# Kernel tuning notes

Measured on AMD Instinct MI355X. Metric: run time of the kernel, lower is better.

## Reference

```python
import jax, jax.numpy as jnp
import numpy as np

V = 128   # vocab / number of symbols (len(index_map))
N = 512   # number of automaton states
L = 4096  # input string length


def setup_inputs() -> dict:
    key = jax.random.key(0)
    k0, k1, k2, k3, k4 = jax.random.split(key, 5)
    tokens = jax.random.randint(k0, (L,), 0, V, dtype=jnp.int32)
    # start distribution over states
    start = jax.nn.softmax(jax.random.normal(k1, (N,), dtype=jnp.float32))
    # row-stochastic transition matrices, one per symbol: [V, N, N]
    transfer = jax.nn.softmax(jax.random.normal(k2, (V, N, N), dtype=jnp.float32), axis=-1)
    # per-symbol prob vectors near 1.0 so the running product stays finite: [V, N]
    probs = 0.9 + 0.2 * jax.random.uniform(k3, (V, N), dtype=jnp.float32)
    # final acceptance vector: [N]
    finals = jax.random.uniform(k4, (N,), dtype=jnp.float32)
    return {"tokens": tokens, "start": start, "transfer": transfer,
            "probs": probs, "finals": finals}


def reference(tokens, start, transfer, probs, finals):
    # Faithful device-side version of the Python loop:
    #   prob *= internal @ prob_tensors[sym]; internal = internal @ transfer_tensors[sym]
    # index_map is identity (symbol == tensor index). Whole walk is one lax.scan,
    # removing the per-step host sync of the original.
    def step(carry, t):
        internal, prob = carry
        prob = prob * jnp.dot(internal, probs[t])          # scalar emission prob
        internal = jnp.dot(internal, transfer[t])          # [N] @ [N,N] -> [N]
        return (internal, prob), None

    init = (start, jnp.float32(1.0))
    (internal, prob), _ = jax.lax.scan(step, init, tokens)
    prob = prob * jnp.dot(internal, finals)
    return internal, prob
```

## Files before the change

### kernel.cpp

```cpp
#include <hip/hip_runtime.h>
#include <stdint.h>


typedef unsigned short ushort_t;
typedef __attribute__((ext_vector_type(8))) short v8s;
typedef __attribute__((ext_vector_type(4))) float f32x4;

#define NSTATE 512
#define NSYM   128
#define LTOK   4096
#define MS     ((size_t)NSTATE*NSTATE)

__device__ __forceinline__ ushort_t f2bf(float f){
  unsigned u = __float_as_uint(f);
  u = u + 0x7FFFu + ((u >> 16) & 1u);
  return (ushort_t)(u >> 16);
}
__device__ __forceinline__ float bf2f(ushort_t h){
  return __uint_as_float(((unsigned)h) << 16);
}
__device__ __forceinline__ size_t fragT_idx(int m, int k){
  return ((size_t)((k >> 5)*512 + m)*4 + ((k >> 3) & 3))*8 + (k & 7);
}

__device__ __forceinline__ void step_mfma64(f32x4 acc[4][4],
    const ushort_t* __restrict__ As, const ushort_t* __restrict__ Bf,
    int wv, int l15, int q4){
  const ushort_t* base = Bf + ((size_t)(wv*64 + l15)*4 + q4)*8;
  v8s aA[4], aN[4];
  #pragma unroll
  for (int mt = 0; mt < 4; ++mt) aA[mt] = *(const v8s*)&base[mt*512];
  #pragma unroll
  for (int kk = 0; kk < 16; ++kk){
    if (kk < 15){
      #pragma unroll
      for (int mt = 0; mt < 4; ++mt)
        aN[mt] = *(const v8s*)&base[(size_t)(kk+1)*16384 + mt*512];
    }
    #pragma unroll
    for (int nt = 0; nt < 4; ++nt){
      int n  = nt*16 + l15;
      int ch = kk*4 + q4;
      v8s bf = *(const v8s*)&As[n*512 + ((ch ^ (n & 7))*8)];
      #pragma unroll
      for (int mt = 0; mt < 4; ++mt)
        acc[mt][nt] = __builtin_amdgcn_mfma_f32_16x16x32_bf16(aA[mt], bf, acc[mt][nt], 0,0,0);
    }
    #pragma unroll
    for (int mt = 0; mt < 4; ++mt) aA[mt] = aN[mt];
  }
}

__device__ __forceinline__ void load_strip64(ushort_t* As,
    const ushort_t* __restrict__ src, int rowbase, int tid){
  #pragma unroll
  for (int q = 0; q < 8; ++q){
    int F = tid + q*512;
    int m = F >> 6, p = F & 63;
    *(v8s*)&As[m*512 + p*8] =
      *(const v8s*)&src[(size_t)(rowbase + m)*NSTATE + ((p ^ (m & 7))*8)];
  }
}

__device__ __forceinline__ void writeback64(ushort_t* As, f32x4 acc[4][4],
    int wv, int l15, int q4){
  #pragma unroll
  for (int nt = 0; nt < 4; ++nt){
    int n = nt*16 + l15;
    #pragma unroll
    for (int mt = 0; mt < 4; ++mt){
      int col = wv*64 + mt*16 + q4*4;
      ushort4 h;
      h.x = f2bf(acc[mt][nt][0]); h.y = f2bf(acc[mt][nt][1]);
      h.z = f2bf(acc[mt][nt][2]); h.w = f2bf(acc[mt][nt][3]);
      int p = (col >> 3) ^ (n & 7);
      *(ushort4*)&As[n*512 + p*8 + (col & 7)] = h;
    }
  }
}

__device__ __forceinline__ void store_out64(ushort_t* slot, f32x4 acc[4][4],
    int rowbase, bool even, int lane, int wv, int l15, int q4){
  if (even){
    #pragma unroll
    for (int nt = 0; nt < 4; ++nt){
      int grow = rowbase + nt*16 + l15;
      #pragma unroll
      for (int mt = 0; mt < 4; ++mt){
        int gcol = wv*64 + mt*16 + q4*4;
        ushort4 h;
        h.x = f2bf(acc[mt][nt][0]); h.y = f2bf(acc[mt][nt][1]);
        h.z = f2bf(acc[mt][nt][2]); h.w = f2bf(acc[mt][nt][3]);
        *(ushort4*)&slot[(size_t)grow*NSTATE + gcol] = h;
      }
    }
  } else {
    #pragma unroll
    for (int nt = 0; nt < 4; ++nt){
      int G0 = rowbase + nt*16 + (l15 & 12);
      #pragma unroll
      for (int mt = 0; mt < 4; ++mt){
        float v0 = acc[mt][nt][0], v1 = acc[mt][nt][1];
        float v2 = acc[mt][nt][2], v3 = acc[mt][nt][3];
        float s0 = __shfl_xor(v0, 2), s1 = __shfl_xor(v1, 2);
        float s2 = __shfl_xor(v2, 2), s3 = __shfl_xor(v3, 2);
        const bool h2 = lane & 2;
        float c0 = h2 ? s2 : v0, c1 = h2 ? s3 : v1;
        float c2 = h2 ? v2 : s0, c3 = h2 ? v3 : s1;
        float u0 = __shfl_xor(c0, 1), u1 = __shfl_xor(c1, 1);
        float u2 = __shfl_xor(c2, 1), u3 = __shfl_xor(c3, 1);
        const bool h1 = lane & 1;
        float d0 = h1 ? u1 : c0, d1 = h1 ? c1 : u0;
        float d2 = h1 ? u3 : c2, d3 = h1 ? c3 : u2;
        int mcol = wv*64 + mt*16 + q4*4 + (lane & 3);
        ushort4 h;
        h.x = f2bf(d0); h.y = f2bf(d1); h.z = f2bf(d2); h.w = f2bf(d3);
        *(ushort4*)&slot[fragT_idx(mcol, G0)] = h;
      }
    }
  }
}

__global__ __launch_bounds__(512, 4) void k_chain3(
    const int* __restrict__ tokens, const ushort_t* __restrict__ Tb,
    const ushort_t* __restrict__ Tf, ushort_t* __restrict__ Lout, int W){
  extern __shared__ __align__(16) ushort_t As[];
  const int b = blockIdx.x;
  const int c       = (b >> 6) * 8 + (b & 7);
  const int rowbase = ((b >> 3) & 7) * 64;
  const int tid  = threadIdx.x;
  const int lane = tid & 63;
  const int wv   = tid >> 6;
  const int l15  = lane & 15;
  const int q4   = lane >> 4;
  const int t0   = c * W;

  load_strip64(As, Tb + (size_t)tokens[t0] * MS, rowbase, tid);
  __syncthreads();
  for (int k = 1; k < W; ++k){
    f32x4 acc[4][4];
    #pragma unroll
    for (int mt = 0; mt < 4; ++mt)
      #pragma unroll
      for (int nt = 0; nt < 4; ++nt) acc[mt][nt] = (f32x4){0.f,0.f,0.f,0.f};
    step_mfma64(acc, As, Tf + (size_t)tokens[t0 + k] * MS, wv, l15, q4);
    __syncthreads();
    if (k < W - 1){
      writeback64(As, acc, wv, l15, q4);
      __syncthreads();
    } else {
      store_out64(Lout + (size_t)c * MS, acc, rowbase, !(c & 1), lane, wv, l15, q4);
    }
  }
}

__global__ __launch_bounds__(512, 4) void k_tree3(
    const ushort_t* __restrict__ Lsrc, ushort_t* __restrict__ Ldst){
  extern __shared__ __align__(16) ushort_t As[];
  const int b = blockIdx.x;
  int j, strip;
  if (gridDim.x >= 64){ j = (b >> 6) * 8 + (b & 7); strip = (b >> 3) & 7; }
  else                { j = b >> 3;                  strip = b & 7; }
  const int rowbase = strip * 64;
  const int tid  = threadIdx.x;
  const int lane = tid & 63;
  const int wv   = tid >> 6;
  const int l15  = lane & 15;
  const int q4   = lane >> 4;
  load_strip64(As, Lsrc + (size_t)(2*j) * MS, rowbase, tid);
  __syncthreads();
  f32x4 acc[4][4];
  #pragma unroll
  for (int mt = 0; mt < 4; ++mt)
    #pragma unroll
    for (int nt = 0; nt < 4; ++nt) acc[mt][nt] = (f32x4){0.f,0.f,0.f,0.f};
  step_mfma64(acc, As, Lsrc + (size_t)(2*j + 1) * MS, wv, l15, q4);
  store_out64(Ldst + (size_t)j * MS, acc, rowbase, !(j & 1), lane, wv, l15, q4);
}

__global__ __launch_bounds__(256) void k_prep(const float* __restrict__ transfer,
                                              ushort_t* __restrict__ Tb,
                                              ushort_t* __restrict__ Tf){
  __shared__ ushort_t t[32*512];
  const int s = blockIdx.x >> 4;
  const int kk = blockIdx.x & 15;
  const int krows = kk * 32;
  const int tid = threadIdx.x;
  for (int idx = tid; idx < 32*512; idx += 256){
    int r = idx >> 9, n = idx & 511;
    ushort_t h = f2bf(transfer[(size_t)s*MS + (size_t)(krows + r)*NSTATE + n]);
    Tb[(size_t)s*MS + (size_t)(krows + r)*NSTATE + n] = h;
    t[r*512 + n] = h;
  }
  __syncthreads();
  for (int idx = tid; idx < 512*4; idx += 256){
    int n = idx >> 2, cc = idx & 3;
    v8s vv;
    #pragma unroll
    for (int jj = 0; jj < 8; ++jj) vv[jj] = (short)t[(cc*8 + jj)*512 + n];
    *(v8s*)&Tf[(size_t)s*MS + ((size_t)(kk*512 + n)*4 + cc)*8] = vv;
  }
}

__device__ __forceinline__ void gl_lds16(const void* g, void* l){
  __builtin_amdgcn_global_load_lds(
      (const __attribute__((address_space(1))) unsigned int*)g,
      (__attribute__((address_space(3))) unsigned int*)l, 16, 0, 0);
}

__device__ void gemm_step(const ushort_t* __restrict__ A,
                          const ushort_t* __restrict__ Bf,
                          ushort_t* dRM, ushort_t* dT, int rowbase){
  __shared__ __align__(16) ushort_t ldsA[128*64];
  __shared__ __align__(16) ushort_t ldsB[128*64];
  const int tid  = threadIdx.x;
  const int lane = tid & 63;
  const int w    = tid >> 6;
  const int l15  = lane & 15;
  const int koff = (lane >> 4) * 8;

  __threadfence_block();

  for (int p = 0; p < 4; ++p){
    f32x4 acc[2][8];
    #pragma unroll
    for (int rt = 0; rt < 2; ++rt)
      #pragma unroll
      for (int ct = 0; ct < 8; ++ct) acc[rt][ct] = (f32x4){0.f,0.f,0.f,0.f};

    for (int kk = 0; kk < 8; ++kk){
      __syncthreads();
      #pragma unroll
      for (int q = 0; q < 4; ++q){
        int idx = tid + q*256;
        int rr = idx >> 3, cch = idx & 7;
        gl_lds16(&A [(size_t)(rowbase + rr)*NSTATE + kk*64 + cch*8], &ldsA[idx*8]);
        gl_lds16(&Bf[fragT_idx(p*128 + rr, kk*64 + cch*8)], &ldsB[idx*8]);
      }
      __syncthreads();
      #pragma unroll
      for (int kc = 0; kc < 2; ++kc){
        v8s a0 = *(const v8s*)&ldsA[(w*32 +      l15)*64 + kc*32 + koff];
        v8s a1 = *(const v8s*)&ldsA[(w*32 + 16 + l15)*64 + kc*32 + koff];
        #pragma unroll
        for (int ct = 0; ct < 8; ++ct){
          v8s bb = *(const v8s*)&ldsB[(ct*16 + l15)*64 + kc*32 + koff];
          acc[0][ct] = __builtin_amdgcn_mfma_f32_16x16x32_bf16(a0, bb, acc[0][ct], 0,0,0);
          acc[1][ct] = __builtin_amdgcn_mfma_f32_16x16x32_bf16(a1, bb, acc[1][ct], 0,0,0);
        }
      }
    }
    const int rb = rowbase + w*32 + (lane >> 4)*4;
    #pragma unroll
    for (int rt = 0; rt < 2; ++rt)
      #pragma unroll
      for (int ct = 0; ct < 8; ++ct)
        #pragma unroll
        for (int i = 0; i < 4; ++i){
          int grow = rb + rt*16 + i;
          int gcol = p*128 + ct*16 + l15;
          ushort_t h = f2bf(acc[rt][ct][i]);
          if (dRM) dRM[(size_t)grow*NSTATE + gcol] = h;
          if (dT)  dT [fragT_idx(gcol, grow)] = h;
        }
  }
  __syncthreads();
}

__global__ __launch_bounds__(256) void k_chain(const int* __restrict__ tokens,
    const ushort_t* __restrict__ Tb, const ushort_t* __restrict__ Tf,
    ushort_t* ping, ushort_t* pong, ushort_t* Lout, int W){
  const int c = blockIdx.x >> 2;
  const int r = blockIdx.x & 3;
  const int t0 = c * W;
  ushort_t* bufA = ping + (size_t)c * MS;
  ushort_t* bufB = pong + (size_t)c * MS;
  for (int k = 1; k < W; ++k){
    const ushort_t* Asrc = (k == 1) ? Tb + (size_t)tokens[t0] * MS
                                    : (((k - 1) & 1) ? bufA : bufB);
    ushort_t *dRM, *dT;
    if (k == W - 1){
      ushort_t* slot = Lout + (size_t)c * MS;
      dRM = (c & 1) ? nullptr : slot;
      dT  = (c & 1) ? slot    : nullptr;
    } else {
      dRM = (k & 1) ? bufA : bufB; dT = nullptr;
    }
    gemm_step(Asrc, Tf + (size_t)tokens[t0 + k] * MS, dRM, dT, r * 128);
  }
}

__global__ __launch_bounds__(256) void k_tree(const ushort_t* __restrict__ Lsrc,
                                              ushort_t* __restrict__ Ldst){
  const int j = blockIdx.x >> 2, r = blockIdx.x & 3;
  const ushort_t* A  = Lsrc + (size_t)(2*j)     * MS;
  const ushort_t* Bf = Lsrc + (size_t)(2*j + 1) * MS;
  ushort_t* slot = Ldst + (size_t)j * MS;
  gemm_step(A, Bf, (j & 1) ? nullptr : slot, (j & 1) ? slot : nullptr, r * 128);
}

__global__ __launch_bounds__(512) void k_descent(const float* __restrict__ start,
    const ushort_t* __restrict__ lvl4, const ushort_t* __restrict__ Upper,
    float* __restrict__ u, int baseLvl){
  __shared__ float v[NSTATE];
  const int upOff[7] = {0,128,192,224,240,248,252};
  const int g = blockIdx.x, tid = threadIdx.x;
  v[tid] = start[tid];
  __syncthreads();
  int pos = 0;
  for (int p = 11 - baseLvl; p >= 0; --p){
    if ((g >> p) & 1){
      const int L = baseLvl + p;
      const ushort_t* arr = (L == 4) ? lvl4 : (Upper + (size_t)upOff[L-5] * MS);
      const ushort_t* M = arr + (size_t)(pos >> p) * MS;
      float a0=0.f,a1=0.f,a2=0.f,a3=0.f;
      #pragma unroll 4
      for (int i = 0; i < NSTATE; i += 4){
        a0 += v[i  ] * bf2f(M[(size_t)(i  )*NSTATE + tid]);
        a1 += v[i+1] * bf2f(M[(size_t)(i+1)*NSTATE + tid]);
        a2 += v[i+2] * bf2f(M[(size_t)(i+2)*NSTATE + tid]);
        a3 += v[i+3] * bf2f(M[(size_t)(i+3)*NSTATE + tid]);
      }
      __syncthreads();
      v[tid] = (a0+a1)+(a2+a3);
      __syncthreads();
      pos += 1 << p;
    }
  }
  u[(size_t)g*NSTATE + tid] = v[tid];
}

__global__ __launch_bounds__(512) void k_phase2(const int* __restrict__ tokens,
    const float* __restrict__ u, const ushort_t* __restrict__ Tf,
    const float* __restrict__ probs, float* __restrict__ partials,
    float* __restrict__ out, int SEG){
  __shared__ float v[NSTATE];
  __shared__ float redc[8], redm[8];
  __shared__ float fac, minv;
  const int g = blockIdx.x, tid = threadIdx.x;
  v[tid] = u[(size_t)g*NSTATE + tid];
  float pp = 1.f;
  __syncthreads();
  for (int k = 0; k < SEG; ++k){
    const int tok = tokens[g*SEG + k];
    float a = v[tid];
    float bb = a * probs[(size_t)tok*NSTATE + tid];
    #pragma unroll
    for (int o = 32; o > 0; o >>= 1){
      a  += __shfl_down(a, o);
      bb += __shfl_down(bb, o);
    }
    if ((tid & 63) == 0){ redm[tid >> 6] = a; redc[tid >> 6] = bb; }
    __syncthreads();
    if (tid == 0){
      float m = 0.f, cc = 0.f;
      #pragma unroll
      for (int q = 0; q < 8; ++q){ m += redm[q]; cc += redc[q]; }
      fac = cc / m;
    }
    __syncthreads();
    pp *= fac;
    const ushort_t* Mf = Tf + (size_t)tok * MS + (size_t)tid * 32;
    float a0=0.f,a1=0.f,a2=0.f,a3=0.f;
    for (int bnd = 0; bnd < 16; ++bnd){
      const v8s* pv = (const v8s*)&Mf[(size_t)bnd*16384];
      v8s h0 = pv[0], h1 = pv[1], h2 = pv[2], h3 = pv[3];
      const float* vb = &v[bnd*32];
      #pragma unroll
      for (int j = 0; j < 8; ++j){
        a0 += vb[j     ] * bf2f((ushort_t)h0[j]);
        a1 += vb[j +  8] * bf2f((ushort_t)h1[j]);
        a2 += vb[j + 16] * bf2f((ushort_t)h2[j]);
        a3 += vb[j + 24] * bf2f((ushort_t)h3[j]);
      }
    }
    __syncthreads();
    v[tid] = (a0+a1)+(a2+a3);
    __syncthreads();
  }
  if (tid == 0) partials[g] = pp;
  if (g == gridDim.x - 1){
    float a = v[tid];
    #pragma unroll
    for (int o = 32; o > 0; o >>= 1) a += __shfl_down(a, o);
    if ((tid & 63) == 0) redm[tid >> 6] = a;
    __syncthreads();
    if (tid == 0){
      float m = 0.f;
      #pragma unroll
      for (int q = 0; q < 8; ++q) m += redm[q];
      minv = 1.f / m;
    }
    __syncthreads();
    out[tid] = v[tid] * minv;
  }
}

__global__ __launch_bounds__(512) void k_finish(const float* __restrict__ partials,
    const float* __restrict__ finals, float* out, int G){
  __shared__ float red[8];
  const int tid = threadIdx.x;
  float x = out[tid] * finals[tid];
  #pragma unroll
  for (int o = 32; o > 0; o >>= 1) x += __shfl_down(x, o);
  if ((tid & 63) == 0) red[tid >> 6] = x;
  __syncthreads();
  if (tid == 0){
    float s = 0.f;
    for (int q = 0; q < 8; ++q) s += red[q];
    float pp = 1.f;
    for (int q = 0; q < G; ++q) pp *= partials[q];
    out[NSTATE] = pp * s;
  }
}

__global__ __launch_bounds__(512) void k_fallback(const int* __restrict__ tokens,
    const float* __restrict__ start, const float* __restrict__ transfer,
    const float* __restrict__ probs, const float* __restrict__ finals,
    float* out){
  __shared__ float v[NSTATE];
  __shared__ float red[9];
  const int tid = threadIdx.x;
  v[tid] = start[tid];
  float pp = 1.f;
  __syncthreads();
  for (int t = 0; t < LTOK; ++t){
    const int tok = tokens[t];
    float x = v[tid] * probs[(size_t)tok*NSTATE + tid];
    #pragma unroll
    for (int o = 32; o > 0; o >>= 1) x += __shfl_down(x, o);
    if ((tid & 63) == 0) red[tid >> 6] = x;
    __syncthreads();
    if (tid == 0){
      float cc = 0.f;
      for (int q = 0; q < 8; ++q) cc += red[q];
      red[8] = cc;
    }
    __syncthreads();
    pp *= red[8];
    const float* M = transfer + (size_t)tok * MS;
    float acc = 0.f;
    #pragma unroll 8
    for (int i = 0; i < NSTATE; ++i) acc += v[i] * M[(size_t)i*NSTATE + tid];
    __syncthreads();
    v[tid] = acc;
    __syncthreads();
  }
  out[tid] = v[tid];
  float x = v[tid] * finals[tid];
  #pragma unroll
  for (int o = 32; o > 0; o >>= 1) x += __shfl_down(x, o);
  if ((tid & 63) == 0) red[tid >> 6] = x;
  __syncthreads();
  if (tid == 0){
    float s = 0.f;
    for (int q = 0; q < 8; ++q) s += red[q];
    out[NSTATE] = pp * s;
  }
}

extern "C" void kernel_launch(void* const* d_in, const int* in_sizes, int n_in,
                              void* d_out, int out_size, void* d_ws, size_t ws_size,
                              hipStream_t stream) {
  const int*   tokens   = (const int*)  d_in[0];
  const float* start    = (const float*)d_in[1];
  const float* transfer = (const float*)d_in[2];
  const float* probs    = (const float*)d_in[3];
  const float* finals   = (const float*)d_in[4];
  float* out = (float*)d_out;
  (void)in_sizes; (void)n_in; (void)out_size;

  const size_t C2 = MS * 2;
  size_t off = 0;
  const size_t o_Tb    = off; off += C2 * NSYM;
  const size_t o_Tf    = off; off += C2 * NSYM;
  const size_t o_Upper = off; off += C2 * 254;
  const size_t o_u     = off; off += (size_t)256 * NSTATE * 4;
  const size_t o_part  = off; off += 256 * 4 + 256;
  const size_t common  = off;

  const int LDSBYTES = 64*512*2;
  bool bigLds =
    hipFuncSetAttribute(reinterpret_cast<const void*>(k_chain3),
        hipFuncAttributeMaxDynamicSharedMemorySize, LDSBYTES) == hipSuccess &&
    hipFuncSetAttribute(reinterpret_cast<const void*>(k_tree3),
        hipFuncAttributeMaxDynamicSharedMemorySize, LDSBYTES) == hipSuccess;

  char* ws = (char*)d_ws;
  ushort_t* Tb    = (ushort_t*)(ws + o_Tb);
  ushort_t* Tf    = (ushort_t*)(ws + o_Tf);
  ushort_t* Upper = (ushort_t*)(ws + o_Upper);
  float*    u     = (float*)   (ws + o_u);
  float*    parts = (float*)   (ws + o_part);

  const int upOff[7] = {0,128,192,224,240,248,252};
  ushort_t* lvl[12] = {nullptr};
  for (int l = 5; l <= 11; ++l) lvl[l] = Upper + (size_t)upOff[l-5] * MS;

  int W = 0, sLvl = 0;
  size_t oo = common;
  if (bigLds){
    if      (ws_size >= common + C2 * (512 + 256)) { W = 8;  sLvl = 3; }
    else if (ws_size >= common + C2 * 256)         { W = 16; sLvl = 4; }
    else if (ws_size >= common)                    { W = 32; sLvl = 5; }
    if (W){
      if (W == 8) { lvl[3] = (ushort_t*)(ws + oo); oo += C2 * 512; }
      if (W <= 16){ lvl[4] = (ushort_t*)(ws + oo); oo += C2 * 256; }
    }
  } else {
    if (ws_size >= common + C2 * 256) { W = 32; sLvl = 5; }
  }
  if (!W){
    k_fallback<<<1, 512, 0, stream>>>(tokens, start, transfer, probs, finals, out);
    return;
  }
  const int nchain = LTOK / W;
  const int G    = lvl[4] ? 256 : 128;
  const int SEGc = LTOK / G;
  const int baseLvl = lvl[4] ? 4 : 5;

  k_prep<<<NSYM * 16, 256, 0, stream>>>(transfer, Tb, Tf);
  if (bigLds){
    k_chain3<<<nchain * 8, 512, LDSBYTES, stream>>>(tokens, Tb, Tf, lvl[sLvl], W);
    for (int l = sLvl; l < 11; ++l){
      const int cntNext = LTOK >> (l + 1);
      k_tree3<<<cntNext * 8, 512, LDSBYTES, stream>>>(lvl[l], lvl[l + 1]);
    }
  } else {
    ushort_t* ping = (ushort_t*)(ws + oo); oo += C2 * nchain;
    ushort_t* pong = (ushort_t*)(ws + oo); oo += C2 * nchain;
    k_chain<<<nchain * 4, 256, 0, stream>>>(tokens, Tb, Tf, ping, pong, lvl[sLvl], W);
    for (int l = sLvl; l < 11; ++l){
      const int cntNext = LTOK >> (l + 1);
      k_tree<<<cntNext * 4, 256, 0, stream>>>(lvl[l], lvl[l + 1]);
    }
  }
  k_descent<<<G, 512, 0, stream>>>(start, lvl[4], Upper, u, baseLvl);
  k_phase2 <<<G, 512, 0, stream>>>(tokens, u, Tf, probs, parts, out, SEGc);
  k_finish <<<1, 512, 0, stream>>>(parts, finals, out, G);
}
```

Before: 1.783 ms.

## Prefetch next step's transfer fragments across chain steps and remap block indices

```diff
diff --git a/kernel.cpp b/kernel.cpp
--- a/kernel.cpp
+++ b/kernel.cpp
@@ -23,24 +23,49 @@
   return ((size_t)((k >> 5)*512 + m)*4 + ((k >> 3) & 3))*8 + (k & 7);
 }
 
-__device__ __forceinline__ void step_mfma64(f32x4 acc[4][4],
-    const ushort_t* __restrict__ As, const ushort_t* __restrict__ Bf,
+
+__device__ __forceinline__ void step_mfma64_pf(f32x4 acc[4][4],
+    const ushort_t* __restrict__ As, const ushort_t* __restrict__ basek,
+    const ushort_t* __restrict__ baseN, v8s aA[4],
     int wv, int l15, int q4){
-  const ushort_t* base = Bf + ((size_t)(wv*64 + l15)*4 + q4)*8;
-  v8s aA[4], aN[4];
-  #pragma unroll
-  for (int mt = 0; mt < 4; ++mt) aA[mt] = *(const v8s*)&base[mt*512];
-  #pragma unroll
-  for (int kk = 0; kk < 16; ++kk){
-    if (kk < 15){
-      #pragma unroll
-      for (int mt = 0; mt < 4; ++mt)
-        aN[mt] = *(const v8s*)&base[(size_t)(kk+1)*16384 + mt*512];
-    }
+  #pragma unroll
+  for (int i = 0; i < 16; ++i){
+    v8s aN[4];
+    const ushort_t* src = (i < 15) ? (basek + (size_t)(i + 1)*16384) : baseN;
+    #pragma unroll
+    for (int mt = 0; mt < 4; ++mt)
+      aN[mt] = *(const v8s*)&src[mt*512];
     #pragma unroll
     for (int nt = 0; nt < 4; ++nt){
       int n  = nt*16 + l15;
-      int ch = kk*4 + q4;
+      int ch = i*4 + q4;
+      v8s bf = *(const v8s*)&As[n*512 + ((ch ^ (n & 7))*8)];
+      #pragma unroll
+      for (int mt = 0; mt < 4; ++mt)
+        acc[mt][nt] = __builtin_amdgcn_mfma_f32_16x16x32_bf16(aA[mt], bf, acc[mt][nt], 0,0,0);
+    }
+    #pragma unroll
+    for (int mt = 0; mt < 4; ++mt) aA[mt] = aN[mt];
+  }
+}
+
+__device__ __forceinline__ void step_mfma64_one(f32x4 acc[4][4],
+    const ushort_t* __restrict__ As, const ushort_t* __restrict__ base,
+    int wv, int l15, int q4){
+  v8s aA[4], aN[4];
+  #pragma unroll
+  for (int mt = 0; mt < 4; ++mt) aA[mt] = *(const v8s*)&base[mt*512];
+  #pragma unroll
+  for (int i = 0; i < 16; ++i){
+    if (i < 15){
+      #pragma unroll
+      for (int mt = 0; mt < 4; ++mt)
+        aN[mt] = *(const v8s*)&base[(size_t)(i + 1)*16384 + mt*512];
+    }
+    #pragma unroll
+    for (int nt = 0; nt < 4; ++nt){
+      int n  = nt*16 + l15;
+      int ch = i*4 + q4;
       v8s bf = *(const v8s*)&As[n*512 + ((ch ^ (n & 7))*8)];
       #pragma unroll
       for (int mt = 0; mt < 4; ++mt)
@@ -125,25 +150,35 @@
     const int* __restrict__ tokens, const ushort_t* __restrict__ Tb,
     const ushort_t* __restrict__ Tf, ushort_t* __restrict__ Lout, int W){
   extern __shared__ __align__(16) ushort_t As[];
-  const int b = blockIdx.x;
-  const int c       = (b >> 6) * 8 + (b & 7);
-  const int rowbase = ((b >> 3) & 7) * 64;
+  const int b   = blockIdx.x;
+  const int o   = b >> 3;
+  const int c   = (o >> 6)*64 + ((o >> 2) & 7)*8 + (b & 7);
+  const int strip = (o & 3)*2 + ((o >> 5) & 1);
+  const int rowbase = strip * 64;
   const int tid  = threadIdx.x;
   const int lane = tid & 63;
   const int wv   = tid >> 6;
   const int l15  = lane & 15;
   const int q4   = lane >> 4;
   const int t0   = c * W;
+  const size_t laneoff = ((size_t)(wv*64 + l15)*4 + q4)*8;
 
   load_strip64(As, Tb + (size_t)tokens[t0] * MS, rowbase, tid);
-  __syncthreads();
+  const ushort_t* basek = Tf + (size_t)tokens[t0 + 1] * MS + laneoff;
+  v8s aA[4];
+  #pragma unroll
+  for (int mt = 0; mt < 4; ++mt) aA[mt] = *(const v8s*)&basek[mt*512];
+  __syncthreads();
+
   for (int k = 1; k < W; ++k){
+    const ushort_t* baseN = (k + 1 < W)
+        ? (Tf + (size_t)tokens[t0 + k + 1] * MS + laneoff) : basek;
     f32x4 acc[4][4];
     #pragma unroll
     for (int mt = 0; mt < 4; ++mt)
       #pragma unroll
       for (int nt = 0; nt < 4; ++nt) acc[mt][nt] = (f32x4){0.f,0.f,0.f,0.f};
-    step_mfma64(acc, As, Tf + (size_t)tokens[t0 + k] * MS, wv, l15, q4);
+    step_mfma64_pf(acc, As, basek, baseN, aA, wv, l15, q4);
     __syncthreads();
     if (k < W - 1){
       writeback64(As, acc, wv, l15, q4);
@@ -151,22 +186,23 @@
     } else {
       store_out64(Lout + (size_t)c * MS, acc, rowbase, !(c & 1), lane, wv, l15, q4);
     }
+    basek = baseN;
   }
 }
 
 __global__ __launch_bounds__(512, 4) void k_tree3(
-    const ushort_t* __restrict__ Lsrc, ushort_t* __restrict__ Ldst){
+    const ushort_t* __restrict__ Lsrc, ushort_t* __restrict__ Ldst, int nodes){
   extern __shared__ __align__(16) ushort_t As[];
   const int b = blockIdx.x;
-  int j, strip;
-  if (gridDim.x >= 64){ j = (b >> 6) * 8 + (b & 7); strip = (b >> 3) & 7; }
-  else                { j = b >> 3;                  strip = b & 7; }
+  const int j = b % nodes;
+  const int strip = b / nodes;
   const int rowbase = strip * 64;
   const int tid  = threadIdx.x;
   const int lane = tid & 63;
   const int wv   = tid >> 6;
   const int l15  = lane & 15;
   const int q4   = lane >> 4;
+  const size_t laneoff = ((size_t)(wv*64 + l15)*4 + q4)*8;
   load_strip64(As, Lsrc + (size_t)(2*j) * MS, rowbase, tid);
   __syncthreads();
   f32x4 acc[4][4];
@@ -174,7 +210,7 @@
   for (int mt = 0; mt < 4; ++mt)
     #pragma unroll
     for (int nt = 0; nt < 4; ++nt) acc[mt][nt] = (f32x4){0.f,0.f,0.f,0.f};
-  step_mfma64(acc, As, Lsrc + (size_t)(2*j + 1) * MS, wv, l15, q4);
+  step_mfma64_one(acc, As, Lsrc + (size_t)(2*j + 1) * MS + laneoff, wv, l15, q4);
   store_out64(Ldst + (size_t)j * MS, acc, rowbase, !(j & 1), lane, wv, l15, q4);
 }
 
@@ -524,7 +560,7 @@
     k_chain3<<<nchain * 8, 512, LDSBYTES, stream>>>(tokens, Tb, Tf, lvl[sLvl], W);
     for (int l = sLvl; l < 11; ++l){
       const int cntNext = LTOK >> (l + 1);
-      k_tree3<<<cntNext * 8, 512, LDSBYTES, stream>>>(lvl[l], lvl[l + 1]);
+      k_tree3<<<cntNext * 8, 512, LDSBYTES, stream>>>(lvl[l], lvl[l + 1], cntNext);
     }
   } else {
     ushort_t* ping = (ushort_t*)(ws + oo); oo += C2 * nchain;
```

Result: no change. 1.800 ms (+0.9%).
